# Kernel tuning notes

Measured on AMD Instinct MI355X. Metric: run time of the kernel, lower is better.

The kernel has to match this reference:

```python
import jax, jax.numpy as jnp
import numpy as np
import math

B, A, S, H = 4, 3, 1024, 768
NH, HD = 12, 64  # num_heads, head_dim
TEMP = 1.0
LN_EPS = 1e-5


def setup_inputs() -> dict:
    key = jax.random.key(0)
    ks = jax.random.split(key, 8)
    w_scale = math.sqrt(6.0 / (H + H))  # xavier_uniform
    def lin_w(k):
        return jax.random.uniform(k, (H, H), jnp.float32, -w_scale, w_scale)
    return {
        "query": jax.random.normal(ks[0], (B, S, H), jnp.float32),
        "adapter_outputs": jax.random.normal(ks[1], (B, A, S, H), jnp.float32),
        "Wq": lin_w(ks[2]), "bq": jnp.zeros((H,), jnp.float32),
        "Wk": lin_w(ks[3]), "bk": jnp.zeros((H,), jnp.float32),
        "Wv": lin_w(ks[4]), "bv": jnp.zeros((H,), jnp.float32),
        "Wo": lin_w(ks[5]), "bo": jnp.zeros((H,), jnp.float32),
        "gamma": jnp.ones((H,), jnp.float32),
        "beta": jnp.zeros((H,), jnp.float32),
    }


def reference(query, adapter_outputs, Wq, bq, Wk, bk, Wv, bv, Wo, bo, gamma, beta):
    # Q: [B,S,H] -> [B,NH,S,HD]
    Q = (query @ Wq.T + bq).reshape(B, S, NH, HD).transpose(0, 2, 1, 3)
    # K,V: [B,A,S,H] -> [B,NH,A,S,HD] (vectorizes the per-adapter torch loop)
    K = (adapter_outputs @ Wk.T + bk).reshape(B, A, S, NH, HD).transpose(0, 3, 1, 2, 4)
    V = (adapter_outputs @ Wv.T + bv).reshape(B, A, S, NH, HD).transpose(0, 3, 1, 2, 4)
    scores = jnp.einsum('bhqd,bhasd->bhqas', Q, K) / (math.sqrt(HD) * TEMP)
    # softmax over the ADAPTER axis only (dim=3), as in the original
    attn = jax.nn.softmax(scores, axis=3)
    # sum over both adapters and source positions
    attended = jnp.einsum('bhqas,bhasd->bhqd', attn, V)
    attended = attended.transpose(0, 2, 1, 3).reshape(B, S, H)
    out = attended @ Wo.T + bo
    x = out + query
    mu = jnp.mean(x, axis=-1, keepdims=True)
    var = jnp.mean(jnp.square(x - mu), axis=-1, keepdims=True)
    out = (x - mu) * jax.lax.rsqrt(var + LN_EPS) * gamma + beta
    avg_weights = attn.mean(axis=1).mean(axis=2)  # [B,Q,S]
    return out, avg_weights
```

## Files before the change

kernel.cpp:

```cpp
#include <hip/hip_runtime.h>

#define NB 4
#define NA 3
#define NS 1024
#define NHID 768
#define NHEADS 12
#define HD 64

typedef __bf16 bf16_t;
typedef __bf16 bf16x8 __attribute__((ext_vector_type(8)));
typedef __bf16 bf16x4 __attribute__((ext_vector_type(4)));
typedef float f32x4 __attribute__((ext_vector_type(4)));

#define MFMA(a, b, c) __builtin_amdgcn_mfma_f32_16x16x32_bf16(a, b, c, 0, 0, 0)

static __device__ __forceinline__ bf16x8 load8(const bf16_t* p) {
    return *reinterpret_cast<const bf16x8*>(p);
}

typedef __attribute__((address_space(3))) unsigned int u32_lds;
typedef __attribute__((address_space(1))) unsigned int u32_glb;
static __device__ __forceinline__ void gl_lds16(const void* g, void* lds_base_uniform) {
    __builtin_amdgcn_global_load_lds((const u32_glb*)g, (u32_lds*)lds_base_uniform, 16, 0, 0);
}

static __device__ __forceinline__ bf16x8 cvt8(f32x4 lo, f32x4 hi) {
    bf16x8 r;
    r[0] = (bf16_t)lo[0]; r[1] = (bf16_t)lo[1]; r[2] = (bf16_t)lo[2]; r[3] = (bf16_t)lo[3];
    r[4] = (bf16_t)hi[0]; r[5] = (bf16_t)hi[1]; r[6] = (bf16_t)hi[2]; r[7] = (bf16_t)hi[3];
    return r;
}


__global__ __launch_bounds__(256) void cvt6(
    const float* __restrict__ s0, bf16_t* __restrict__ d0, int c0,
    const float* __restrict__ s1, bf16_t* __restrict__ d1, int c1,
    const float* __restrict__ s2, bf16_t* __restrict__ d2, int c2,
    const float* __restrict__ s3, bf16_t* __restrict__ d3, int c3,
    const float* __restrict__ s4, bf16_t* __restrict__ d4, int c4,
    const float* __restrict__ s5, bf16_t* __restrict__ d5, int c5)
{
    const int bid = blockIdx.x;
    const float* s; bf16_t* d; int rel;
    if      (bid < c0) { s = s0; d = d0; rel = bid; }
    else if (bid < c1) { s = s1; d = d1; rel = bid - c0; }
    else if (bid < c2) { s = s2; d = d2; rel = bid - c1; }
    else if (bid < c3) { s = s3; d = d3; rel = bid - c2; }
    else if (bid < c4) { s = s4; d = d4; rel = bid - c3; }
    else               { s = s5; d = d5; rel = bid - c4; }
    const int t = threadIdx.x;
#pragma unroll
    for (int k = 0; k < 4; k++) {
        size_t u = (size_t)rel * 1024 + k * 256 + t;
        f32x4 v = reinterpret_cast<const f32x4*>(s)[u];
        bf16x4 o;
        o[0] = (bf16_t)v[0]; o[1] = (bf16_t)v[1];
        o[2] = (bf16_t)v[2]; o[3] = (bf16_t)v[3];
        reinterpret_cast<bf16x4*>(d)[u] = o;
    }
}

template <int WMODE, int NT>
__global__ __launch_bounds__(64) void wgemm(
    const bf16_t* __restrict__ X,
    const bf16_t* __restrict__ W0, const bf16_t* __restrict__ W1,
    const float* __restrict__ bias0, const float* __restrict__ bias1,
    const float* __restrict__ resid,
    bf16_t* __restrict__ out0, bf16_t* __restrict__ outV,
    float* __restrict__ outf,
    const bf16_t* __restrict__ X2, const bf16_t* __restrict__ W2,
    const float* __restrict__ bias2, bf16_t* __restrict__ out2)
{
    __shared__ __align__(16) char smem[2][8192];

    const int lane = threadIdx.x & 63;
    const int quad = lane >> 4, l15 = lane & 15;

    int emode = (WMODE == 4) ? 1 : WMODE;
    int nt    = NT;
    int bid   = blockIdx.x;
    const bf16_t* Xp = X;
    const bf16_t* Wp = W0;
    const float*  b0 = bias0;
    bf16_t*       o0 = out0;
    if constexpr (WMODE == 4) {
        if (bid >= 4608) {
            emode = 0; nt = 12; bid -= 4608;
            Xp = X2; Wp = W2; b0 = bias2; o0 = out2;
        }
    }
    const int xcd = bid & 7, jj = bid >> 3;
    const int n_t = jj % nt, slab = jj / nt;
    const int m0 = (slab * 8 + xcd) * 64;
    const int n0 = n_t * 64;

    const bf16_t* Wsel = (emode == 1 && n0 >= 768) ? W1 : Wp;
    const int n0b = (emode == 1 && n0 >= 768) ? n0 - 768 : n0;

    const bf16_t* Ap[4];
    const bf16_t* Bp[4];
#pragma unroll
    for (int i = 0; i < 4; i++) {
        Ap[i] = Xp   + (size_t)(m0  + i * 16 + l15) * NHID + quad * 8;
        Bp[i] = Wsel + (size_t)(n0b + i * 16 + l15) * NHID + quad * 8;
    }
    auto stage = [&](char* base) {
#pragma unroll
        for (int i = 0; i < 4; i++) { gl_lds16(Ap[i], base + i * 1024);        Ap[i] += 32; }
#pragma unroll
        for (int i = 0; i < 4; i++) { gl_lds16(Bp[i], base + 4096 + i * 1024); Bp[i] += 32; }
    };

    f32x4 acc[4][4];
#pragma unroll
    for (int i = 0; i < 4; i++)
#pragma unroll
        for (int j = 0; j < 4; j++) acc[i][j] = 0.0f;

    constexpr int KITER = NHID / 32;
    stage(smem[0]);
    stage(smem[1]);

    for (int it = 0; it < KITER; ++it) {
        if (it == KITER - 1) asm volatile("s_waitcnt vmcnt(0)" ::: "memory");
        else                 asm volatile("s_waitcnt vmcnt(8)" ::: "memory");
        char* cur = smem[it & 1];
        bf16x8 af[4], bfr[4];
#pragma unroll
        for (int i = 0; i < 4; i++) af[i]  = *(const bf16x8*)(cur + (i * 64 + lane) * 16);
#pragma unroll
        for (int j = 0; j < 4; j++) bfr[j] = *(const bf16x8*)(cur + 4096 + (j * 64 + lane) * 16);
        asm volatile("s_waitcnt lgkmcnt(0)" ::: "memory");
        if (it + 2 < KITER) stage(cur);
#pragma unroll
        for (int i = 0; i < 4; i++)
#pragma unroll
            for (int j = 0; j < 4; j++)
                acc[i][j] = MFMA(af[i], bfr[j], acc[i][j]);
    }

    if (emode == 1 && n0 >= 768) {
        char* img = smem[0];
        const int hh  = (n0 - 768) >> 6;
        const int b   = m0 / (NA * NS);
        const int rem = m0 - b * (NA * NS);
        const int a   = rem >> 10;
        const int s0  = rem & 1023;
#pragma unroll
        for (int i = 0; i < 4; i++) {
#pragma unroll
            for (int j = 0; j < 4; j++) {
                float bn = bias1[(n0 - 768) + j * 16 + l15];
                bf16x4 pk;
#pragma unroll
                for (int rg = 0; rg < 4; rg++) pk[rg] = (bf16_t)(acc[i][j][rg] + bn);
                int off = (i >> 1) * 4096 + j * 1024 + (quad * 16 + l15) * 16 + (i & 1) * 8;
                *reinterpret_cast<bf16x4*>(img + off) = pk;
            }
        }
        asm volatile("s_waitcnt lgkmcnt(0)" ::: "memory");
        char* gbase = (char*)outV + (size_t)((b * NHEADS + hh) * NA + a) * 131072
                      + (size_t)(s0 >> 5) * 4096;
#pragma unroll
        for (int p = 0; p < 8; p++) {
            f32x4 v = *reinterpret_cast<const f32x4*>(img + p * 1024 + lane * 16);
            *reinterpret_cast<f32x4*>(gbase + p * 1024 + lane * 16) = v;
        }
    } else {
#pragma unroll
        for (int i = 0; i < 4; i++) {
#pragma unroll
            for (int j = 0; j < 4; j++) {
                const int n = n0 + j * 16 + l15;
                const float bn = b0[n];
#pragma unroll
                for (int rg = 0; rg < 4; rg++) {
                    const int m = m0 + i * 16 + quad * 4 + rg;
                    float v = acc[i][j][rg] + bn;
                    if (emode == 0) {
                        int b = m >> 10, s = m & 1023, hh = n >> 6, d = n & 63;
                        o0[(((size_t)(b * NHEADS + hh) * NS) + s) * HD + d] = (bf16_t)v;
                    } else if (emode == 1) {
                        int b = m / (NA * NS);
                        int rem = m - b * (NA * NS);
                        int a = rem >> 10, s = rem & 1023;
                        int hh = n >> 6, d = n & 63;
                        o0[((((size_t)(b * NHEADS + hh) * NA + a) * NS) + s) * HD + d] = (bf16_t)v;
                    } else {
                        v += resid[(size_t)m * NHID + n];
                        outf[(size_t)m * NHID + n] = v;
                    }
                }
            }
        }
    }
}

template <int MODE, int NT, bool ABF, bool BBF>
__global__ __launch_bounds__(256) void proj_gemm(
    const void* __restrict__ Xv,
    const void* __restrict__ W0v, const void* __restrict__ W1v,
    const float* __restrict__ bias0, const float* __restrict__ bias1,
    const float* __restrict__ resid,
    bf16_t* __restrict__ out0, bf16_t* __restrict__ out1,
    float* __restrict__ outf)
{
    constexpr int ASZ   = ABF ? 8192 : 16384;
    constexpr int BSZ   = BBF ? 8192 : 16384;
    constexpr int BUFSZ = ASZ + BSZ;
    constexpr int LPS   = (ABF ? 2 : 4) + (BBF ? 2 : 4);
    __shared__ __align__(16) char smem[3 * BUFSZ];

    const int t = threadIdx.x;
    const int lane = t & 63, w = t >> 6;
    const int quad = lane >> 4, l15 = lane & 15;
    const int wm = w >> 1, wn = w & 1;

    const int bid = blockIdx.x;
    const int xcd = bid & 7, jj = bid >> 3;
    const int n_t = jj % NT, slab = jj / NT;
    const int m0 = (slab * 8 + xcd) * 128;
    const int n0 = n_t * 128;

    const void* Wselv = (MODE == 1 && n0 >= 768) ? W1v : W0v;
    const int n0b = (MODE == 1 && n0 >= 768) ? n0 - 768 : n0;

    const int srow  = lane >> 3;
    const int schnk = (lane & 7) ^ srow;
    const float*  Apf[4];
    const bf16_t* Apb[2];
    const float*  Bpf[4];
    const bf16_t* Bpb[2];
    if constexpr (ABF) {
        const bf16_t* X = (const bf16_t*)Xv;
#pragma unroll
        for (int i = 0; i < 2; i++) {
            int g = w * 2 + i;
            Apb[i] = X + (size_t)(m0 + g * 16 + l15) * NHID + quad * 8;
        }
    } else {
        const float* X = (const float*)Xv;
#pragma unroll
        for (int i = 0; i < 4; i++) {
            int g = w * 4 + i;
            Apf[i] = X + (size_t)(m0 + g * 8 + srow) * NHID + schnk * 4;
        }
    }
    if constexpr (BBF) {
        const bf16_t* Wb = (const bf16_t*)Wselv;
#pragma unroll
        for (int i = 0; i < 2; i++) {
            int g = w * 2 + i;
            Bpb[i] = Wb + (size_t)(n0b + g * 16 + l15) * NHID + quad * 8;
        }
    } else {
        const float* Wf = (const float*)Wselv;
#pragma unroll
        for (int i = 0; i < 4; i++) {
            int g = w * 4 + i;
            Bpf[i] = Wf + (size_t)(n0b + g * 8 + srow) * NHID + schnk * 4;
        }
    }

    auto stage = [&](char* base) {
        char* Ab = base;
        char* Bb = base + ASZ;
        if constexpr (ABF) {
#pragma unroll
            for (int i = 0; i < 2; i++) { gl_lds16(Apb[i], Ab + (w * 2 + i) * 1024); Apb[i] += 32; }
        } else {
#pragma unroll
            for (int i = 0; i < 4; i++) { gl_lds16(Apf[i], Ab + (w * 4 + i) * 1024); Apf[i] += 32; }
        }
        if constexpr (BBF) {
#pragma unroll
            for (int i = 0; i < 2; i++) { gl_lds16(Bpb[i], Bb + (w * 2 + i) * 1024); Bpb[i] += 32; }
        } else {
#pragma unroll
            for (int i = 0; i < 4; i++) { gl_lds16(Bpf[i], Bb + (w * 4 + i) * 1024); Bpf[i] += 32; }
        }
    };

    auto wait_one = [&]() {
        if constexpr (LPS == 4)      asm volatile("s_waitcnt vmcnt(4)" ::: "memory");
        else if constexpr (LPS == 6) asm volatile("s_waitcnt vmcnt(6)" ::: "memory");
        else                         asm volatile("s_waitcnt vmcnt(8)" ::: "memory");
    };

    f32x4 acc[4][4];
#pragma unroll
    for (int i = 0; i < 4; i++)
#pragma unroll
        for (int j = 0; j < 4; j++) acc[i][j] = 0.0f;

    constexpr int KITER = NHID / 32;
    stage(smem);
    stage(smem + BUFSZ);
    int put = 2, get = 0;

    for (int it = 0; it < KITER; ++it) {
        if (it == KITER - 1) asm volatile("s_waitcnt vmcnt(0)" ::: "memory");
        else                 wait_one();
        __builtin_amdgcn_s_barrier();
        if (it + 2 < KITER) {
            stage(smem + put * BUFSZ);
            put = (put == 2) ? 0 : put + 1;
        }

        char* Ab = smem + get * BUFSZ;
        char* Bb = Ab + ASZ;
        get = (get == 2) ? 0 : get + 1;

        bf16x8 af[4], bfr[4];
        const int pl = (2 * quad) ^ (l15 & 7);
#pragma unroll
        for (int i = 0; i < 4; i++) {
            if constexpr (ABF) {
                int mt = wm * 4 + i;
                af[i] = *(const bf16x8*)(Ab + (mt * 64 + lane) * 16);
            } else {
                int R = (wm * 4 + i) * 16 + l15;
                f32x4 lo = *(const f32x4*)(Ab + R * 128 + pl * 16);
                f32x4 hi = *(const f32x4*)(Ab + R * 128 + (pl ^ 1) * 16);
                af[i] = cvt8(lo, hi);
            }
        }
#pragma unroll
        for (int j = 0; j < 4; j++) {
            if constexpr (BBF) {
                int ntj = wn * 4 + j;
                bfr[j] = *(const bf16x8*)(Bb + (ntj * 64 + lane) * 16);
            } else {
                int R = (wn * 4 + j) * 16 + l15;
                f32x4 lo = *(const f32x4*)(Bb + R * 128 + pl * 16);
                f32x4 hi = *(const f32x4*)(Bb + R * 128 + (pl ^ 1) * 16);
                bfr[j] = cvt8(lo, hi);
            }
        }
#pragma unroll
        for (int i = 0; i < 4; i++)
#pragma unroll
            for (int j = 0; j < 4; j++)
                acc[i][j] = MFMA(af[i], bfr[j], acc[i][j]);
    }

#pragma unroll
    for (int i = 0; i < 4; i++) {
#pragma unroll
        for (int j = 0; j < 4; j++) {
            const int n = n0 + wn * 64 + j * 16 + l15;
            float bn;
            if (MODE == 1) bn = (n < 768) ? bias0[n] : bias1[n - 768];
            else           bn = bias0[n];
            if (MODE == 1 && n >= 768) {
                const int m = m0 + wm * 64 + i * 16 + quad * 4;
                int b = m / (NA * NS);
                int rem = m - b * (NA * NS);
                int a = rem >> 10, s = rem & 1023;
                int hh = (n - 768) >> 6;
                bf16x4 pk;
#pragma unroll
                for (int rg = 0; rg < 4; rg++) pk[rg] = (bf16_t)(acc[i][j][rg] + bn);
                char* dst = (char*)out1 + (size_t)((b * NHEADS + hh) * NA + a) * 131072
                            + (size_t)(s >> 5) * 4096 + j * 1024
                            + (quad * 16 + l15) * 16 + (i & 1) * 8;
                *reinterpret_cast<bf16x4*>(dst) = pk;
            } else {
#pragma unroll
                for (int rg = 0; rg < 4; rg++) {
                    const int m = m0 + wm * 64 + i * 16 + quad * 4 + rg;
                    float v = acc[i][j][rg] + bn;
                    if (MODE == 0) {
                        int b = m >> 10, s = m & 1023, hh = n >> 6, d = n & 63;
                        out0[(((size_t)(b * NHEADS + hh) * NS) + s) * HD + d] = (bf16_t)v;
                    } else if (MODE == 1) {
                        int b = m / (NA * NS);
                        int rem = m - b * (NA * NS);
                        int a = rem >> 10, s = rem & 1023;
                        int hh = n >> 6, d = n & 63;
                        out0[((((size_t)(b * NHEADS + hh) * NA + a) * NS) + s) * HD + d] = (bf16_t)v;
                    } else {
                        v += resid[(size_t)m * NHID + n];
                        outf[(size_t)m * NHID + n] = v;
                    }
                }
            }
        }
    }
}

__global__ __launch_bounds__(256, 3) void attn_kernel(
    const bf16_t* __restrict__ Q, const bf16_t* __restrict__ K,
    const bf16_t* __restrict__ VT, bf16_t* __restrict__ AT)
{
    __shared__ __align__(16) char kv[2 * 24576];

    const int t    = threadIdx.x;
    const int w    = t >> 6, lane = t & 63;
    const int quad = lane >> 4, l15 = lane & 15;

    int bh, qt;
    if (gridDim.x == 768) {
        int xcd = blockIdx.x & 7, j = blockIdx.x >> 3;
        bh = (j >> 4) * 8 + xcd;
        qt = ((j & 15) << 2) | w;
    } else {
        bh = blockIdx.x >> 4;
        qt = ((blockIdx.x & 15) << 2) | w;
    }
    const int b  = bh / NHEADS, h = bh - b * NHEADS;
    const int q0 = qt * 16;

    const bf16_t* Qb = Q + ((size_t)bh * NS + q0) * HD;
    bf16x8 qf0 = load8(Qb + l15 * HD + quad * 8);
    bf16x8 qf1 = load8(Qb + l15 * HD + quad * 8 + 32);

    const char* gp[6];
    int gdelta[6], loff[6];
#pragma unroll
    for (int i = 0; i < 6; i++) {
        int g = w * 6 + i;
        loff[i] = g >= 12 ? 12288 + (g - 12) * 1024 : g * 1024;
        if (g < 12) {
            int a = g >> 2, j = (g >> 1) & 1, dh = g & 1;
            gp[i] = (const char*)(K + ((size_t)(bh * NA + a) * NS + j * 16 + l15) * HD
                                  + dh * 32 + quad * 8);
            gdelta[i] = 32 * HD * 2;
        } else {
            int gi = g - 12;
            int a = gi >> 2, dt = gi & 3;
            gp[i] = (const char*)VT + (size_t)(bh * NA + a) * 131072
                    + dt * 1024 + (size_t)lane * 16;
            gdelta[i] = 4096;
        }
    }

    auto stage = [&](int buf) {
#pragma unroll
        for (int i = 0; i < 6; i++) {
            gl_lds16(gp[i], kv + buf * 24576 + loff[i]);
            gp[i] += gdelta[i];
        }
    };

    f32x4 acc[4];
#pragma unroll
    for (int dt = 0; dt < 4; dt++) acc[dt] = 0.0f;

    const float KS = 0.18033688011112042f;

    stage(0);
    __syncthreads();

    for (int it = 0; it < 32; ++it) {
        if (it + 1 < 32) stage((it + 1) & 1);

        const char* base = kv + (it & 1) * 24576;
        f32x4 sc[3][2];
#pragma unroll
        for (int a = 0; a < 3; a++) {
#pragma unroll
            for (int j = 0; j < 2; j++) {
                bf16x8 klo = *(const bf16x8*)(base + ((a * 4 + j * 2 + 0) * 64 + lane) * 16);
                bf16x8 khi = *(const bf16x8*)(base + ((a * 4 + j * 2 + 1) * 64 + lane) * 16);
                f32x4 z = 0.0f;
                f32x4 c0 = MFMA(klo, qf0, z);
                sc[a][j] = MFMA(khi, qf1, c0);
            }
        }
        f32x4 plo[3], phi[3];
#pragma unroll
        for (int j = 0; j < 2; j++) {
#pragma unroll
            for (int rg = 0; rg < 4; rg++) {
                float x0 = sc[0][j][rg], x1 = sc[1][j][rg], x2 = sc[2][j][rg];
                float mx = fmaxf(x0, fmaxf(x1, x2));
                float e0 = __builtin_amdgcn_exp2f((x0 - mx) * KS);
                float e1 = __builtin_amdgcn_exp2f((x1 - mx) * KS);
                float e2 = __builtin_amdgcn_exp2f((x2 - mx) * KS);
                float inv = __builtin_amdgcn_rcpf(e0 + e1 + e2);
                if (j == 0) {
                    plo[0][rg] = e0 * inv; plo[1][rg] = e1 * inv; plo[2][rg] = e2 * inv;
                } else {
                    phi[0][rg] = e0 * inv; phi[1][rg] = e1 * inv; phi[2][rg] = e2 * inv;
                }
            }
        }
#pragma unroll
        for (int a = 0; a < 3; a++) {
            bf16x8 pf = cvt8(plo[a], phi[a]);
#pragma unroll
            for (int dt = 0; dt < 4; dt++) {
                bf16x8 vf = *(const bf16x8*)(base + 12288 + ((a * 4 + dt) * 64 + lane) * 16);
                acc[dt] = MFMA(pf, vf, acc[dt]);
            }
        }
        __syncthreads();
    }

    bf16_t* Ob = AT + (size_t)b * NS * NHID;
#pragma unroll
    for (int dt = 0; dt < 4; dt++) {
#pragma unroll
        for (int rg = 0; rg < 4; rg++) {
            int qq = q0 + quad * 4 + rg;
            Ob[(size_t)qq * NHID + h * HD + dt * 16 + l15] = (bf16_t)acc[dt][rg];
        }
    }
}

__global__ __launch_bounds__(256) void ln_kernel(
    float* __restrict__ X, const float* __restrict__ gamma,
    const float* __restrict__ beta)
{
    const int row = blockIdx.x;
    const int t = threadIdx.x;
    float* x = X + (size_t)row * NHID;
    float v0 = x[t], v1 = x[t + 256], v2 = x[t + 512];
    float s  = v0 + v1 + v2;
    float s2 = v0 * v0 + v1 * v1 + v2 * v2;
#pragma unroll
    for (int off = 32; off > 0; off >>= 1) {
        s  += __shfl_down(s, off);
        s2 += __shfl_down(s2, off);
    }
    __shared__ float red[8];
    const int w = t >> 6, lane = t & 63;
    if (lane == 0) { red[w] = s; red[4 + w] = s2; }
    __syncthreads();
    s  = red[0] + red[1] + red[2] + red[3];
    s2 = red[4] + red[5] + red[6] + red[7];
    float mu  = s * (1.0f / NHID);
    float var = s2 * (1.0f / NHID) - mu * mu;
    float rs  = rsqrtf(fmaxf(var, 0.0f) + 1e-5f);
    x[t]       = (v0 - mu) * rs * gamma[t]       + beta[t];
    x[t + 256] = (v1 - mu) * rs * gamma[t + 256] + beta[t + 256];
    x[t + 512] = (v2 - mu) * rs * gamma[t + 512] + beta[t + 512];
}

__global__ __launch_bounds__(256) void fill_third(float* __restrict__ p)
{
    const int i = blockIdx.x * 256 + threadIdx.x;
    f32x4 v = { 1.0f / 3.0f, 1.0f / 3.0f, 1.0f / 3.0f, 1.0f / 3.0f };
    *reinterpret_cast<f32x4*>(p + (size_t)i * 4) = v;
}

extern "C" void kernel_launch(void* const* d_in, const int* in_sizes, int n_in,
                              void* d_out, int out_size, void* d_ws, size_t ws_size,
                              hipStream_t stream)
{
    (void)in_sizes; (void)n_in; (void)out_size;
    const float* query = (const float*)d_in[0];
    const float* adapt = (const float*)d_in[1];
    const float* Wq    = (const float*)d_in[2];
    const float* bq    = (const float*)d_in[3];
    const float* Wk    = (const float*)d_in[4];
    const float* bk    = (const float*)d_in[5];
    const float* Wv    = (const float*)d_in[6];
    const float* bv    = (const float*)d_in[7];
    const float* Wo    = (const float*)d_in[8];
    const float* bo    = (const float*)d_in[9];
    const float* gamma = (const float*)d_in[10];
    const float* beta  = (const float*)d_in[11];

    float*  out0  = (float*)d_out;
    float*  out1f = out0 + 3145728;
    bf16_t* out1b = (bf16_t*)out1f;

    dim3 blk(256);

    if (ws_size >= (size_t)67633152) {
        bf16_t* Kw  = (bf16_t*)d_ws;
        bf16_t* VTw = (bf16_t*)((char*)d_ws + 18874368);
        bf16_t* Adb = (bf16_t*)((char*)d_ws + 37748736);
        bf16_t* Wqb = (bf16_t*)((char*)d_ws + 56623104);
        bf16_t* Wkb = (bf16_t*)((char*)d_ws + 57802752);
        bf16_t* Wvb = (bf16_t*)((char*)d_ws + 58982400);
        bf16_t* Wob = (bf16_t*)((char*)d_ws + 60162048);
        bf16_t* Qcb = (bf16_t*)((char*)d_ws + 61341696);
        bf16_t* Qw  = out1b;
        bf16_t* ATw = out1b + 3145728;
        cvt6<<<dim3(3648), blk, 0, stream>>>(
            adapt, Adb, 2304, query, Qcb, 3072,
            Wq, Wqb, 3216, Wk, Wkb, 3360, Wv, Wvb, 3504, Wo, Wob, 3648);
        wgemm<4, 24><<<dim3(5376), dim3(64), 0, stream>>>(
            Adb, Wkb, Wvb, bk, bv, nullptr, Kw, VTw, nullptr,
            Qcb, Wqb, bq, Qw);
        attn_kernel<<<dim3(768), blk, 0, stream>>>(Qw, Kw, VTw, ATw);
        wgemm<3, 12><<<dim3(768), dim3(64), 0, stream>>>(
            ATw, Wob, nullptr, bo, nullptr, query, nullptr, nullptr, out0,
            nullptr, nullptr, nullptr, nullptr);
    } else if (ws_size >= (size_t)37748736) {
        bf16_t* Kw  = (bf16_t*)d_ws;
        bf16_t* VTw = (bf16_t*)((char*)d_ws + 18874368);
        bf16_t* Qw  = out1b;
        bf16_t* ATw = out1b + 3145728;
        bf16_t* Wqb = out1b + 6291456;
        bf16_t* Wkb = Wqb + 589824;
        bf16_t* Wvb = Wkb + 589824;
        cvt6<<<dim3(432), blk, 0, stream>>>(
            Wq, Wqb, 144, Wk, Wkb, 288, Wv, Wvb, 432,
            Wv, Wvb, 432, Wv, Wvb, 432, Wv, Wvb, 432);
        proj_gemm<0, 6, false, true><<<dim3(192), blk, 0, stream>>>(
            query, Wqb, nullptr, bq, nullptr, nullptr, Qw, nullptr, nullptr);
        proj_gemm<1, 12, false, true><<<dim3(1152), blk, 0, stream>>>(
            adapt, Wkb, Wvb, bk, bv, nullptr, Kw, VTw, nullptr);
        attn_kernel<<<dim3(768), blk, 0, stream>>>(Qw, Kw, VTw, ATw);
        proj_gemm<3, 6, true, false><<<dim3(192), blk, 0, stream>>>(
            ATw, Wo, nullptr, bo, nullptr, query, nullptr, nullptr, out0);
    } else {
        bf16_t* Qc  = out1b;
        bf16_t* ATc = out1b + 786432;
        bf16_t* Kc  = out1b + 1572864;
        bf16_t* VTc = out1b + 3932160;
        for (int b = 0; b < NB; b++) {
            const float* qb = query + (size_t)b * NS * NHID;
            const float* ab = adapt + (size_t)b * NA * NS * NHID;
            proj_gemm<0, 6, false, false><<<dim3(48), blk, 0, stream>>>(
                qb, Wq, nullptr, bq, nullptr, nullptr, Qc, nullptr, nullptr);
            proj_gemm<1, 12, false, false><<<dim3(288), blk, 0, stream>>>(
                ab, Wk, Wv, bk, bv, nullptr, Kc, VTc, nullptr);
            attn_kernel<<<dim3(192), blk, 0, stream>>>(Qc, Kc, VTc, ATc);
            proj_gemm<3, 6, true, false><<<dim3(48), blk, 0, stream>>>(
                ATc, Wo, nullptr, bo, nullptr, qb, nullptr, nullptr,
                out0 + (size_t)b * NS * NHID);
        }
    }

    ln_kernel<<<dim3(4096), blk, 0, stream>>>(out0, gamma, beta);
    fill_third<<<dim3(4096), blk, 0, stream>>>(out1f);
}
```

Measured before the change: 326.3 us.

## Replace single-wave K/V/Q GEMM with 8-wave 256x128 tiled, triple-buffered kernel

Replaces the 64-thread, 64x64-tile wgemm for the fused K/V/Q projection with an 8-wave block computing 256x128 tiles from a triple-buffered LDS pipeline with 64-wide K steps, barriers and MFMA priority raising. The aim is more operand reuse per global load and better latency hiding. The output projection now uses proj_gemm with bf16 inputs, and proj_gemm plus the attention kernel switch to double buffering with explicit vmcnt waits and raw barriers instead of __syncthreads. The V transposed writes now go straight to global instead of through an LDS image, which may coalesce less well. The larger LDS footprint (144KB) limits occupancy to one block per CU.

Measured after the change: 284.4 us. -12.8%, faster.

```diff
diff --git a/kernel.cpp b/kernel.cpp
--- a/kernel.cpp
+++ b/kernel.cpp
@@ -60,55 +60,62 @@
     }
 }
 
-template <int WMODE, int NT>
-__global__ __launch_bounds__(64) void wgemm(
+__global__ __launch_bounds__(512) void gemm8(
     const bf16_t* __restrict__ X,
     const bf16_t* __restrict__ W0, const bf16_t* __restrict__ W1,
     const float* __restrict__ bias0, const float* __restrict__ bias1,
-    const float* __restrict__ resid,
-    bf16_t* __restrict__ out0, bf16_t* __restrict__ outV,
-    float* __restrict__ outf,
+    bf16_t* __restrict__ outK, bf16_t* __restrict__ outV,
     const bf16_t* __restrict__ X2, const bf16_t* __restrict__ W2,
-    const float* __restrict__ bias2, bf16_t* __restrict__ out2)
+    const float* __restrict__ bias2, bf16_t* __restrict__ outQ)
 {
-    __shared__ __align__(16) char smem[2][8192];
-
-    const int lane = threadIdx.x & 63;
+    constexpr int BUFSZ = 49152;
+    __shared__ __align__(16) char smem[3 * BUFSZ];
+
+    const int t = threadIdx.x;
+    const int lane = t & 63, w = t >> 6;
     const int quad = lane >> 4, l15 = lane & 15;
-
-    int emode = (WMODE == 4) ? 1 : WMODE;
-    int nt    = NT;
-    int bid   = blockIdx.x;
+    const int wm = w >> 1, wn = w & 1;
+
+    int emode = 1, nt = 12, bid = blockIdx.x;
     const bf16_t* Xp = X;
     const bf16_t* Wp = W0;
     const float*  b0 = bias0;
-    bf16_t*       o0 = out0;
-    if constexpr (WMODE == 4) {
-        if (bid >= 4608) {
-            emode = 0; nt = 12; bid -= 4608;
-            Xp = X2; Wp = W2; b0 = bias2; o0 = out2;
-        }
-    }
+    if (bid >= 576) {
+        emode = 0; nt = 6; bid -= 576;
+        Xp = X2; Wp = W2; b0 = bias2;
+    }
+
     const int xcd = bid & 7, jj = bid >> 3;
     const int n_t = jj % nt, slab = jj / nt;
-    const int m0 = (slab * 8 + xcd) * 64;
-    const int n0 = n_t * 64;
+    const int m0 = (slab * 8 + xcd) * 256;
+    const int n0 = n_t * 128;
 
     const bf16_t* Wsel = (emode == 1 && n0 >= 768) ? W1 : Wp;
     const int n0b = (emode == 1 && n0 >= 768) ? n0 - 768 : n0;
 
-    const bf16_t* Ap[4];
-    const bf16_t* Bp[4];
-#pragma unroll
-    for (int i = 0; i < 4; i++) {
-        Ap[i] = Xp   + (size_t)(m0  + i * 16 + l15) * NHID + quad * 8;
-        Bp[i] = Wsel + (size_t)(n0b + i * 16 + l15) * NHID + quad * 8;
-    }
-    auto stage = [&](char* base) {
-#pragma unroll
-        for (int i = 0; i < 4; i++) { gl_lds16(Ap[i], base + i * 1024);        Ap[i] += 32; }
-#pragma unroll
-        for (int i = 0; i < 4; i++) { gl_lds16(Bp[i], base + 4096 + i * 1024); Bp[i] += 32; }
+    const bf16_t* sp[6];
+    int loff[6];
+#pragma unroll
+    for (int i = 0; i < 6; i++) {
+        int g = w * 6 + i;
+        loff[i] = g * 1024;
+        if (g < 32) {
+            int ks = g >> 4, mt = g & 15;
+            sp[i] = Xp + (size_t)(m0 + mt * 16 + l15) * NHID + ks * 32 + quad * 8;
+        } else {
+            int gb = g - 32;
+            int ks = gb >> 3, ntile = gb & 7;
+            sp[i] = Wsel + (size_t)(n0b + ntile * 16 + l15) * NHID + ks * 32 + quad * 8;
+        }
+    }
+
+    auto stage_half = [&](char* base, int h) {
+#pragma unroll
+        for (int i = 0; i < 3; i++) {
+            int idx = h * 3 + i;
+            gl_lds16(sp[idx], base + loff[idx]);
+            sp[idx] += 64;
+        }
     };
 
     f32x4 acc[4][4];
@@ -117,78 +124,75 @@
 #pragma unroll
         for (int j = 0; j < 4; j++) acc[i][j] = 0.0f;
 
-    constexpr int KITER = NHID / 32;
-    stage(smem[0]);
-    stage(smem[1]);
+    constexpr int KITER = NHID / 64;
+    stage_half(smem, 0);          stage_half(smem, 1);
+    stage_half(smem + BUFSZ, 0);  stage_half(smem + BUFSZ, 1);
 
     for (int it = 0; it < KITER; ++it) {
         if (it == KITER - 1) asm volatile("s_waitcnt vmcnt(0)" ::: "memory");
-        else                 asm volatile("s_waitcnt vmcnt(8)" ::: "memory");
-        char* cur = smem[it & 1];
-        bf16x8 af[4], bfr[4];
-#pragma unroll
-        for (int i = 0; i < 4; i++) af[i]  = *(const bf16x8*)(cur + (i * 64 + lane) * 16);
-#pragma unroll
-        for (int j = 0; j < 4; j++) bfr[j] = *(const bf16x8*)(cur + 4096 + (j * 64 + lane) * 16);
-        asm volatile("s_waitcnt lgkmcnt(0)" ::: "memory");
-        if (it + 2 < KITER) stage(cur);
-#pragma unroll
-        for (int i = 0; i < 4; i++)
+        else                 asm volatile("s_waitcnt vmcnt(6)" ::: "memory");
+        __builtin_amdgcn_s_barrier();
+
+        const char* rb = smem + (it % 3) * BUFSZ;
+        char* pb = smem + ((it + 2) % 3) * BUFSZ;
+        const bool dostage = (it + 2 < KITER);
+
+#pragma unroll
+        for (int ks = 0; ks < 2; ++ks) {
+            bf16x8 af[4], bfr[4];
+#pragma unroll
+            for (int i = 0; i < 4; i++)
+                af[i] = *(const bf16x8*)(rb + (ks * 16 + wm * 4 + i) * 1024 + lane * 16);
 #pragma unroll
             for (int j = 0; j < 4; j++)
-                acc[i][j] = MFMA(af[i], bfr[j], acc[i][j]);
-    }
-
-    if (emode == 1 && n0 >= 768) {
-        char* img = smem[0];
-        const int hh  = (n0 - 768) >> 6;
-        const int b   = m0 / (NA * NS);
-        const int rem = m0 - b * (NA * NS);
-        const int a   = rem >> 10;
-        const int s0  = rem & 1023;
-#pragma unroll
-        for (int i = 0; i < 4; i++) {
-#pragma unroll
-            for (int j = 0; j < 4; j++) {
-                float bn = bias1[(n0 - 768) + j * 16 + l15];
+                bfr[j] = *(const bf16x8*)(rb + 32768 + (ks * 8 + wn * 4 + j) * 1024 + lane * 16);
+            if (dostage) stage_half(pb, ks);
+            __builtin_amdgcn_s_setprio(1);
+#pragma unroll
+            for (int i = 0; i < 4; i++)
+#pragma unroll
+                for (int j = 0; j < 4; j++)
+                    acc[i][j] = MFMA(af[i], bfr[j], acc[i][j]);
+            __builtin_amdgcn_s_setprio(0);
+            if (ks == 0) __builtin_amdgcn_s_barrier();
+        }
+    }
+
+#pragma unroll
+    for (int i = 0; i < 4; i++) {
+#pragma unroll
+        for (int j = 0; j < 4; j++) {
+            const int n = n0 + wn * 64 + j * 16 + l15;
+            float bn;
+            if (emode == 1) bn = (n < 768) ? b0[n] : bias1[n - 768];
+            else            bn = b0[n];
+            if (emode == 1 && n >= 768) {
+                const int m = m0 + wm * 64 + i * 16 + quad * 4;
+                int b = m / (NA * NS);
+                int rem = m - b * (NA * NS);
+                int a = rem >> 10, s = rem & 1023;
+                int hh = (n - 768) >> 6;
                 bf16x4 pk;
 #pragma unroll
                 for (int rg = 0; rg < 4; rg++) pk[rg] = (bf16_t)(acc[i][j][rg] + bn);
-                int off = (i >> 1) * 4096 + j * 1024 + (quad * 16 + l15) * 16 + (i & 1) * 8;
-                *reinterpret_cast<bf16x4*>(img + off) = pk;
-            }
-        }
-        asm volatile("s_waitcnt lgkmcnt(0)" ::: "memory");
-        char* gbase = (char*)outV + (size_t)((b * NHEADS + hh) * NA + a) * 131072
-                      + (size_t)(s0 >> 5) * 4096;
-#pragma unroll
-        for (int p = 0; p < 8; p++) {
-            f32x4 v = *reinterpret_cast<const f32x4*>(img + p * 1024 + lane * 16);
-            *reinterpret_cast<f32x4*>(gbase + p * 1024 + lane * 16) = v;
-        }
-    } else {
-#pragma unroll
-        for (int i = 0; i < 4; i++) {
-#pragma unroll
-            for (int j = 0; j < 4; j++) {
-                const int n = n0 + j * 16 + l15;
-                const float bn = b0[n];
+                char* dst = (char*)outV + (size_t)((b * NHEADS + hh) * NA + a) * 131072
+                            + (size_t)(s >> 5) * 4096 + j * 1024
+                            + (quad * 16 + l15) * 16 + (i & 1) * 8;
+                *reinterpret_cast<bf16x4*>(dst) = pk;
+            } else {
 #pragma unroll
                 for (int rg = 0; rg < 4; rg++) {
-                    const int m = m0 + i * 16 + quad * 4 + rg;
+                    const int m = m0 + wm * 64 + i * 16 + quad * 4 + rg;
                     float v = acc[i][j][rg] + bn;
                     if (emode == 0) {
                         int b = m >> 10, s = m & 1023, hh = n >> 6, d = n & 63;
-                        o0[(((size_t)(b * NHEADS + hh) * NS) + s) * HD + d] = (bf16_t)v;
-                    } else if (emode == 1) {
+                        outQ[(((size_t)(b * NHEADS + hh) * NS) + s) * HD + d] = (bf16_t)v;
+                    } else {
                         int b = m / (NA * NS);
                         int rem = m - b * (NA * NS);
                         int a = rem >> 10, s = rem & 1023;
                         int hh = n >> 6, d = n & 63;
-                        o0[((((size_t)(b * NHEADS + hh) * NA + a) * NS) + s) * HD + d] = (bf16_t)v;
-                    } else {
-                        v += resid[(size_t)m * NHID + n];
-                        outf[(size_t)m * NHID + n] = v;
+                        outK[((((size_t)(b * NHEADS + hh) * NA + a) * NS) + s) * HD + d] = (bf16_t)v;
                     }
                 }
             }
@@ -209,7 +213,7 @@
     constexpr int BSZ   = BBF ? 8192 : 16384;
     constexpr int BUFSZ = ASZ + BSZ;
     constexpr int LPS   = (ABF ? 2 : 4) + (BBF ? 2 : 4);
-    __shared__ __align__(16) char smem[3 * BUFSZ];
+    __shared__ __align__(16) char smem[2 * BUFSZ];
 
     const int t = threadIdx.x;
     const int lane = t & 63, w = t >> 6;
@@ -295,21 +299,18 @@
 
     constexpr int KITER = NHID / 32;
     stage(smem);
-    stage(smem + BUFSZ);
-    int put = 2, get = 0;
 
     for (int it = 0; it < KITER; ++it) {
-        if (it == KITER - 1) asm volatile("s_waitcnt vmcnt(0)" ::: "memory");
-        else                 wait_one();
+        if (it + 1 < KITER) {
+            stage(smem + ((it + 1) & 1) * BUFSZ);
+            wait_one();
+        } else {
+            asm volatile("s_waitcnt vmcnt(0)" ::: "memory");
+        }
         __builtin_amdgcn_s_barrier();
-        if (it + 2 < KITER) {
-            stage(smem + put * BUFSZ);
-            put = (put == 2) ? 0 : put + 1;
-        }
-
-        char* Ab = smem + get * BUFSZ;
+
+        char* Ab = smem + (it & 1) * BUFSZ;
         char* Bb = Ab + ASZ;
-        get = (get == 2) ? 0 : get + 1;
 
         bf16x8 af[4], bfr[4];
         const int pl = (2 * quad) ^ (l15 & 7);
@@ -342,6 +343,7 @@
 #pragma unroll
             for (int j = 0; j < 4; j++)
                 acc[i][j] = MFMA(af[i], bfr[j], acc[i][j]);
+        __builtin_amdgcn_s_barrier();
     }
 
 #pragma unroll
@@ -450,10 +452,15 @@
     const float KS = 0.18033688011112042f;
 
     stage(0);
-    __syncthreads();
 
     for (int it = 0; it < 32; ++it) {
-        if (it + 1 < 32) stage((it + 1) & 1);
+        if (it + 1 < 32) {
+            stage((it + 1) & 1);
+            asm volatile("s_waitcnt vmcnt(6)" ::: "memory");
+        } else {
+            asm volatile("s_waitcnt vmcnt(0)" ::: "memory");
+        }
+        __builtin_amdgcn_s_barrier();
 
         const char* base = kv + (it & 1) * 24576;
         f32x4 sc[3][2];
@@ -495,7 +502,7 @@
                 acc[dt] = MFMA(pf, vf, acc[dt]);
             }
         }
-        __syncthreads();
+        __builtin_amdgcn_s_barrier();
     }
 
     bf16_t* Ob = AT + (size_t)b * NS * NHID;
@@ -583,13 +590,11 @@
         cvt6<<<dim3(3648), blk, 0, stream>>>(
             adapt, Adb, 2304, query, Qcb, 3072,
             Wq, Wqb, 3216, Wk, Wkb, 3360, Wv, Wvb, 3504, Wo, Wob, 3648);
-        wgemm<4, 24><<<dim3(5376), dim3(64), 0, stream>>>(
-            Adb, Wkb, Wvb, bk, bv, nullptr, Kw, VTw, nullptr,
-            Qcb, Wqb, bq, Qw);
+        gemm8<<<dim3(672), dim3(512), 0, stream>>>(
+            Adb, Wkb, Wvb, bk, bv, Kw, VTw, Qcb, Wqb, bq, Qw);
         attn_kernel<<<dim3(768), blk, 0, stream>>>(Qw, Kw, VTw, ATw);
-        wgemm<3, 12><<<dim3(768), dim3(64), 0, stream>>>(
-            ATw, Wob, nullptr, bo, nullptr, query, nullptr, nullptr, out0,
-            nullptr, nullptr, nullptr, nullptr);
+        proj_gemm<3, 6, true, true><<<dim3(192), blk, 0, stream>>>(
+            ATw, Wob, nullptr, bo, nullptr, query, nullptr, nullptr, out0);
     } else if (ws_size >= (size_t)37748736) {
         bf16_t* Kw  = (bf16_t*)d_ws;
         bf16_t* VTw = (bf16_t*)((char*)d_ws + 18874368);
```
